# Optimization experiments

Measured on AMD Instinct MI355X. Metric: run time of the kernel, lower is better.

The kernel has to match this reference:

```python
import jax, jax.numpy as jnp
import numpy as np

NUM_LEVELS = 4
RADIUS = 4


def _bilinear_zeros(img, x, y):
    """Bilinear sample img (N,H,W) at absolute pixel coords x,y (N,S,S),
    zeros padding outside, matching torch grid_sample(align_corners=True,
    padding_mode='zeros') with absolute->normalized->absolute roundtrip."""
    N, H, W = img.shape
    x0 = jnp.floor(x); y0 = jnp.floor(y)
    x1 = x0 + 1.0;     y1 = y0 + 1.0
    wx1 = x - x0; wx0 = 1.0 - wx1
    wy1 = y - y0; wy0 = 1.0 - wy1
    flat = img.reshape(N, H * W)

    def gather(xi, yi):
        valid = (xi >= 0) & (xi <= W - 1) & (yi >= 0) & (yi <= H - 1)
        xc = jnp.clip(xi, 0, W - 1).astype(jnp.int32)
        yc = jnp.clip(yi, 0, H - 1).astype(jnp.int32)
        idx = (yc * W + xc).reshape(N, -1)
        v = jnp.take_along_axis(flat, idx, axis=1).reshape(xi.shape)
        return jnp.where(valid, v, jnp.zeros((), img.dtype))

    return (wy0 * wx0 * gather(x0, y0) + wy0 * wx1 * gather(x1, y0)
            + wy1 * wx0 * gather(x0, y1) + wy1 * wx1 * gather(x1, y1))


def _avg_pool2(v):
    N, H, W = v.shape
    return v.reshape(N, H // 2, 2, W // 2, 2).mean(axis=(2, 4))


def setup_inputs() -> dict:
    key = jax.random.key(0)
    k1, k2, k3 = jax.random.split(key, 3)
    B, M, C, H, W = 2, 4096, 256, 64, 64
    fmap1 = jax.random.normal(k1, (B, M, C), dtype=jnp.float32)
    fmap2 = jax.random.normal(k2, (B, C, H, W), dtype=jnp.float32)
    u = jax.random.uniform(k3, (B, M, 2), dtype=jnp.float32)
    centroids_coords = u * jnp.array([W - 1, H - 1], dtype=jnp.float32)
    return {"fmap1": fmap1, "fmap2": fmap2, "centroids_coords": centroids_coords}


def reference(fmap1, fmap2, centroids_coords):
    B, M, C = fmap1.shape
    _, _, H, W = fmap2.shape
    side = 2 * RADIUS + 1

    # correlation volume: (B, M, H, W) -> (B*M, H, W)
    corr = jnp.einsum('bmc,bchw->bmhw', fmap1, fmap2).reshape(B * M, H, W)

    d = jnp.arange(-RADIUS, RADIUS + 1, dtype=centroids_coords.dtype)
    di, dj = jnp.meshgrid(d, d, indexing='ij')
    delta = jnp.stack([di, dj], axis=-1)  # (S, S, 2): ch0 = x-offset, ch1 = y-offset

    c = centroids_coords.reshape(B * M, 1, 1, 2)
    vol = corr
    feats = []
    for lvl in range(NUM_LEVELS):
        sc = c + delta                        # (B*M, S, S, 2)
        sampled = _bilinear_zeros(vol, sc[..., 0], sc[..., 1])
        feats.append(sampled.reshape(B, M, side * side))
        c = c / 2.0
        if lvl < NUM_LEVELS - 1:
            vol = _avg_pool2(vol)
    # (B, M, num_levels*S*S) -> (B, out_channels, M)
    return jnp.concatenate(feats, axis=-1).transpose(0, 2, 1)
```

## Files before the change

kernel.cpp:

```cpp
#include <hip/hip_runtime.h>
#include <stdint.h>
#include <stddef.h>

static constexpr int Bb = 2;
static constexpr int Mq = 4096;
static constexpr int Cc = 256;
static constexpr int Hh = 64, Ww = 64;
static constexpr int Np = Hh * Ww;
static constexpr int RAD = 4;
static constexpr int SIDE = 2 * RAD + 1;
static constexpr int KPL = SIDE * SIDE;
static constexpr int NLVL = 4;
static constexpr int KTOT = NLVL * KPL;

static constexpr size_t L1BUF_OFF  = 0;
static constexpr size_t WINBUF_OFF = (size_t)Bb * Mq * 1024;

typedef float floatx4 __attribute__((ext_vector_type(4)));
typedef short shortx8 __attribute__((ext_vector_type(8)));

union BfPack {
    shortx8 v;
    unsigned short u[8];
};

__device__ __forceinline__ unsigned short f2bf(float f) {
    unsigned int x = __float_as_uint(f);
    x += 0x7fffu + ((x >> 16) & 1u);
    return (unsigned short)(x >> 16);
}

__device__ __forceinline__ int ksw(int row, int g) {
    return 8 * (g ^ ((row >> 1) & 3));
}

__global__ __launch_bounds__(256)
void corr_gemm_pool_kernel(const float* __restrict__ A,
                           const float* __restrict__ B2,
                           const float* __restrict__ cent,
                           float* __restrict__ l1buf,
                           float* __restrict__ winbuf)
{
    __shared__ unsigned short la[128 * 32];
    __shared__ unsigned short lb[128 * 32];
    __shared__ float corrT[32 * 129];
    __shared__ int   qx0s[128], qy0s[128];

    const int b    = blockIdx.z;
    const int bm0  = blockIdx.y * 128;
    const int bx   = blockIdx.x;
    const int bn0  = bx * 128;
    const int tid  = threadIdx.x;
    const int lane = tid & 63;
    const int wave = tid >> 6;
    const int lane15 = lane & 15;
    const int quad   = lane >> 4;
    const int wm = (wave >> 1) * 64;
    const int wn = (wave & 1) * 64;

    if (tid < 128) {
        const float cx = cent[(size_t)(b * Mq + bm0 + tid) * 2 + 0];
        const float cy = cent[(size_t)(b * Mq + bm0 + tid) * 2 + 1];
        qx0s[tid] = (int)floorf(cx) - RAD;
        qy0s[tid] = (int)floorf(cy) - RAD;
    }

    const float* Abase = A + (size_t)(b * Mq + bm0) * Cc;
    const float* Bbase = B2 + (size_t)b * Cc * Np + bn0;

    floatx4 acc[4][4];
#pragma unroll
    for (int i = 0; i < 4; ++i)
#pragma unroll
        for (int j = 0; j < 4; ++j)
            acc[i][j] = floatx4{0.0f, 0.0f, 0.0f, 0.0f};

    const int a_row = tid >> 2;
    const int a_g   = tid & 3;
    const int b_n   = tid & 127;
    const int b_g0  = tid >> 7;

    for (int k0 = 0; k0 < Cc; k0 += 32) {
        __syncthreads();
#pragma unroll
        for (int r = 0; r < 2; ++r) {
            const int row = a_row + r * 64;
            const float* src = Abase + (size_t)row * Cc + k0 + a_g * 8;
            const float4 v0 = *(const float4*)(src);
            const float4 v1 = *(const float4*)(src + 4);
            BfPack p;
            p.u[0] = f2bf(v0.x); p.u[1] = f2bf(v0.y);
            p.u[2] = f2bf(v0.z); p.u[3] = f2bf(v0.w);
            p.u[4] = f2bf(v1.x); p.u[5] = f2bf(v1.y);
            p.u[6] = f2bf(v1.z); p.u[7] = f2bf(v1.w);
            *(shortx8*)&la[row * 32 + ksw(row, a_g)] = p.v;
        }
#pragma unroll
        for (int r = 0; r < 2; ++r) {
            const int g = b_g0 + r * 2;
            const float* src = Bbase + (size_t)(k0 + g * 8) * Np + b_n;
            BfPack p;
#pragma unroll
            for (int u = 0; u < 8; ++u)
                p.u[u] = f2bf(src[(size_t)u * Np]);
            *(shortx8*)&lb[b_n * 32 + ksw(b_n, g)] = p.v;
        }
        __syncthreads();
        shortx8 af[4], bf[4];
#pragma unroll
        for (int i = 0; i < 4; ++i) {
            const int row = wm + i * 16 + lane15;
            af[i] = *(const shortx8*)&la[row * 32 + ksw(row, quad)];
        }
#pragma unroll
        for (int j = 0; j < 4; ++j) {
            const int nn = wn + j * 16 + lane15;
            bf[j] = *(const shortx8*)&lb[nn * 32 + ksw(nn, quad)];
        }
#pragma unroll
        for (int i = 0; i < 4; ++i)
#pragma unroll
            for (int j = 0; j < 4; ++j)
                acc[i][j] = __builtin_amdgcn_mfma_f32_16x16x32_bf16(
                    af[i], bf[j], acc[i][j], 0, 0, 0);
    }

    const int m_local = tid >> 3;
    const int xi      = tid & 7;
#pragma unroll
    for (int c = 0; c < 4; ++c) {
        __syncthreads();
        if ((wave >> 1) == (c >> 1)) {
#pragma unroll
            for (int ii = 0; ii < 2; ++ii) {
                const int i = 2 * (c & 1) + ii;
#pragma unroll
                for (int j = 0; j < 4; ++j) {
#pragma unroll
                    for (int reg = 0; reg < 4; ++reg) {
                        const int rl = ii * 16 + quad * 4 + reg;
                        const int n  = wn + j * 16 + lane15;
                        corrT[rl * 129 + n] = acc[i][j][reg];
                    }
                }
            }
        }
        __syncthreads();

        const int mg = 32 * c + m_local;
        const size_t gq = (size_t)(b * Mq + bm0 + mg);
        const float* T = &corrT[m_local * 129];

#pragma unroll
        for (int k = 0; k < 4; ++k) {
            const int c1 = xi + 8 * k;
            const float v = 0.25f * (T[2 * c1] + T[2 * c1 + 1]
                                   + T[64 + 2 * c1] + T[64 + 2 * c1 + 1]);
            l1buf[gq * 1024 + bx * 32 + c1] = v;
        }

        const int x0w = qx0s[mg];
        const int y0w = qy0s[mg];
#pragma unroll
        for (int par = 0; par < 2; ++par) {
            const int wy = 2 * bx + par - y0w;
            if (wy >= 0 && wy < 10) {
#pragma unroll
                for (int t = 0; t < 2; ++t) {
                    const int wx = xi + t * 8;
                    if (wx < 10) {
                        const int x = x0w + wx;
                        if (x >= 0 && x < Ww)
                            winbuf[gq * 100 + wy * 10 + wx] = T[par * 64 + x];
                    }
                }
            }
        }
    }
}

__global__ __launch_bounds__(256)
void pyr_sample_kernel(const float* __restrict__ cent,
                       const float* __restrict__ l1buf,
                       const float* __restrict__ winbuf,
                       float* __restrict__ out)
{
    __shared__ float l1[8][1024];
    __shared__ float l2[8][256];
    __shared__ float l3[8][64];
    __shared__ float win0[8][100];
    __shared__ float qcx[8], qcy[8];
    __shared__ int   qx0[8], qy0[8];

    const int tid = threadIdx.x;
    const int b   = blockIdx.x >> 9;
    const int m0  = (blockIdx.x & 511) * 8;
    const size_t gq0 = (size_t)(b * Mq + m0);

    if (tid < 8) {
        const float cx = cent[(gq0 + tid) * 2 + 0];
        const float cy = cent[(gq0 + tid) * 2 + 1];
        qcx[tid] = cx; qcy[tid] = cy;
        qx0[tid] = (int)floorf(cx) - RAD;
        qy0[tid] = (int)floorf(cy) - RAD;
    }

#pragma unroll
    for (int it = 0; it < 8; ++it) {
        const int v = it * 256 + tid;
        const int q = v >> 8;
        const int o = v & 255;
        *(float4*)&l1[q][o * 4] = *(const float4*)&l1buf[(gq0 + q) * 1024 + o * 4];
    }
    if (tid < 200) {
        const int q = tid / 25;
        const int o = tid - q * 25;
        *(float4*)&win0[q][o * 4] = *(const float4*)&winbuf[(gq0 + q) * 100 + o * 4];
    }
    __syncthreads();

#pragma unroll
    for (int i = 0; i < 8; ++i) {
        const int idx = i * 256 + tid;
        const int q = idx >> 8;
        const int c = idx & 255;
        const int cy2 = c >> 4, cx2 = c & 15;
        const float* s = &l1[q][(2 * cy2) * 32 + 2 * cx2];
        l2[q][c] = 0.25f * (s[0] + s[1] + s[32] + s[33]);
    }
    __syncthreads();
#pragma unroll
    for (int i = 0; i < 2; ++i) {
        const int idx = i * 256 + tid;
        const int q = idx >> 6;
        const int c = idx & 63;
        const int cy3 = c >> 3, cx3 = c & 7;
        const float* s = &l2[q][(2 * cy3) * 16 + 2 * cx3];
        l3[q][c] = 0.25f * (s[0] + s[1] + s[16] + s[17]);
    }
    __syncthreads();

    for (int i = 0; i < 11; ++i) {
        const int idx = i * 256 + tid;
        if (idx >= KTOT * 8) break;
        const int q  = idx & 7;
        const int kk = idx >> 3;
        const int lvl = kk / KPL;
        const int r   = kk - lvl * KPL;
        const int di  = r / SIDE;
        const int dj  = r - di * SIDE;

        const int w = Ww >> lvl;
        const float scale = 1.0f / (float)(1 << lvl);
        const float x = qcx[q] * scale + (float)(di - RAD);
        const float y = qcy[q] * scale + (float)(dj - RAD);

        const float x0f = floorf(x), y0f = floorf(y);
        const float wx1 = x - x0f, wx0 = 1.0f - wx1;
        const float wy1 = y - y0f, wy0 = 1.0f - wy1;
        const float fmx = (float)(w - 1);
        const bool vx0 = (x0f >= 0.0f) && (x0f <= fmx);
        const bool vx1 = (x0f + 1.0f >= 0.0f) && (x0f + 1.0f <= fmx);
        const bool vy0 = (y0f >= 0.0f) && (y0f <= fmx);
        const bool vy1 = (y0f + 1.0f >= 0.0f) && (y0f + 1.0f <= fmx);

        const int ix0 = (int)x0f, iy0 = (int)y0f;

        const float* buf;
        int stride, ox, oy;
        if (lvl == 0)      { buf = win0[q]; stride = 10; ox = qx0[q]; oy = qy0[q]; }
        else if (lvl == 1) { buf = l1[q];   stride = 32; ox = 0; oy = 0; }
        else if (lvl == 2) { buf = l2[q];   stride = 16; ox = 0; oy = 0; }
        else               { buf = l3[q];   stride =  8; ox = 0; oy = 0; }

        const int cx0 = ix0 - ox, cx1 = ix0 + 1 - ox;
        const int cy0r = iy0 - oy, cy1r = iy0 + 1 - oy;
        const float g00 = (vx0 && vy0) ? buf[cy0r * stride + cx0] : 0.0f;
        const float g10 = (vx1 && vy0) ? buf[cy0r * stride + cx1] : 0.0f;
        const float g01 = (vx0 && vy1) ? buf[cy1r * stride + cx0] : 0.0f;
        const float g11 = (vx1 && vy1) ? buf[cy1r * stride + cx1] : 0.0f;

        out[((size_t)b * KTOT + kk) * Mq + m0 + q] =
            wy0 * (wx0 * g00 + wx1 * g10) + wy1 * (wx0 * g01 + wx1 * g11);
    }
}

extern "C" void kernel_launch(void* const* d_in, const int* in_sizes, int n_in,
                              void* d_out, int out_size, void* d_ws, size_t ws_size,
                              hipStream_t stream)
{
    const float* fmap1 = (const float*)d_in[0];
    const float* fmap2 = (const float*)d_in[1];
    const float* cent  = (const float*)d_in[2];
    float* l1buf  = (float*)d_ws + L1BUF_OFF;
    float* winbuf = (float*)d_ws + WINBUF_OFF;
    float* out = (float*)d_out;

    dim3 ggrid(Np / 128, Mq / 128, Bb);
    corr_gemm_pool_kernel<<<ggrid, 256, 0, stream>>>(fmap1, fmap2, cent,
                                                     l1buf, winbuf);

    const int nblk = Bb * Mq / 8;
    pyr_sample_kernel<<<nblk, 256, 0, stream>>>(cent, l1buf, winbuf, out);
}
```

Before: 129.0 us.

## Pre-convert inputs to bf16 and stream GEMM tiles via global_load_lds

Adds two pre-pass kernels that convert fmap1 to bf16 and transpose-convert fmap2 to a K-contiguous bf16 layout in workspace. The GEMM then loads tiles directly into LDS with global_load_lds instead of doing per-element strided fp32 loads and conversions in every block, which were repeated across many blocks. LDS for the staging tiles and the corrT transpose buffer is unioned, and the corrT stride changes. The cost is two extra launches and extra workspace traffic, and the XOR swizzle on the LDS tiles is dropped, which may bring back bank conflicts on the fragment reads.

```diff
diff --git a/kernel.cpp b/kernel.cpp
--- a/kernel.cpp
+++ b/kernel.cpp
@@ -13,8 +13,10 @@
 static constexpr int NLVL = 4;
 static constexpr int KTOT = NLVL * KPL;
 
-static constexpr size_t L1BUF_OFF  = 0;
-static constexpr size_t WINBUF_OFF = (size_t)Bb * Mq * 1024;
+static constexpr size_t L1BUF_B  = 0;
+static constexpr size_t WINBUF_B = (size_t)Bb * Mq * 1024 * 4;
+static constexpr size_t ABF_B    = WINBUF_B + (size_t)Bb * Mq * 100 * 4;
+static constexpr size_t BT_B     = ABF_B + (size_t)Bb * Mq * Cc * 2;
 
 typedef float floatx4 __attribute__((ext_vector_type(4)));
 typedef short shortx8 __attribute__((ext_vector_type(8)));
@@ -30,21 +32,68 @@
     return (unsigned short)(x >> 16);
 }
 
-__device__ __forceinline__ int ksw(int row, int g) {
-    return 8 * (g ^ ((row >> 1) & 3));
+__device__ __forceinline__ void gll16(const void* g, void* l) {
+    __builtin_amdgcn_global_load_lds(
+        (const __attribute__((address_space(1))) unsigned int*)g,
+        (__attribute__((address_space(3))) unsigned int*)l, 16, 0, 0);
 }
 
 __global__ __launch_bounds__(256)
-void corr_gemm_pool_kernel(const float* __restrict__ A,
-                           const float* __restrict__ B2,
+void cvt_a_kernel(const float* __restrict__ in, unsigned short* __restrict__ out)
+{
+    const int t = blockIdx.x * blockDim.x + threadIdx.x;
+    const float4 v0 = *(const float4*)(in + (size_t)t * 8);
+    const float4 v1 = *(const float4*)(in + (size_t)t * 8 + 4);
+    BfPack p;
+    p.u[0] = f2bf(v0.x); p.u[1] = f2bf(v0.y);
+    p.u[2] = f2bf(v0.z); p.u[3] = f2bf(v0.w);
+    p.u[4] = f2bf(v1.x); p.u[5] = f2bf(v1.y);
+    p.u[6] = f2bf(v1.z); p.u[7] = f2bf(v1.w);
+    *(shortx8*)(out + (size_t)t * 8) = p.v;
+}
+
+__global__ __launch_bounds__(256)
+void cvt_bt_kernel(const float* __restrict__ in, unsigned short* __restrict__ out)
+{
+    __shared__ float tile[64 * 65];
+    const int p0 = blockIdx.x * 64;
+    const int c0 = blockIdx.y * 64;
+    const int b  = blockIdx.z;
+    const int tid = threadIdx.x;
+
+    const int pl = tid & 63;
+    const int cb = tid >> 6;
+#pragma unroll
+    for (int it = 0; it < 16; ++it) {
+        const int cl = it * 4 + cb;
+        tile[cl * 65 + pl] = in[((size_t)(b * Cc + c0 + cl)) * Np + p0 + pl];
+    }
+    __syncthreads();
+
+    const int cg = (tid & 7) * 8;
+#pragma unroll
+    for (int it = 0; it < 2; ++it) {
+        const int pw = it * 32 + (tid >> 3);
+        BfPack p;
+#pragma unroll
+        for (int u = 0; u < 8; ++u)
+            p.u[u] = f2bf(tile[(cg + u) * 65 + pw]);
+        *(shortx8*)(out + ((size_t)(b * Np + p0 + pw)) * Cc + c0 + cg) = p.v;
+    }
+}
+
+__global__ __launch_bounds__(256)
+void corr_gemm_pool_kernel(const unsigned short* __restrict__ Abf,
+                           const unsigned short* __restrict__ Bt,
                            const float* __restrict__ cent,
                            float* __restrict__ l1buf,
                            float* __restrict__ winbuf)
 {
-    __shared__ unsigned short la[128 * 32];
-    __shared__ unsigned short lb[128 * 32];
-    __shared__ float corrT[32 * 129];
-    __shared__ int   qx0s[128], qy0s[128];
+    __shared__ union {
+        struct { unsigned short la[128 * 32]; unsigned short lb[128 * 32]; } t;
+        float corrT[32 * 130];
+    } sm;
+    __shared__ int qx0s[128], qy0s[128];
 
     const int b    = blockIdx.z;
     const int bm0  = blockIdx.y * 128;
@@ -65,8 +114,13 @@
         qy0s[tid] = (int)floorf(cy) - RAD;
     }
 
-    const float* Abase = A + (size_t)(b * Mq + bm0) * Cc;
-    const float* Bbase = B2 + (size_t)b * Cc * Np + bn0;
+    unsigned short* la = sm.t.la;
+    unsigned short* lb = sm.t.lb;
+
+    const int lrow = lane >> 2;
+    const int lkg  = (lane & 3) * 8;
+    const unsigned short* aptr = Abf + (size_t)(b * Mq + bm0 + wave * 16 + lrow) * Cc + lkg;
+    const unsigned short* bptr = Bt  + (size_t)(b * Np + bn0 + wave * 16 + lrow) * Cc + lkg;
 
     floatx4 acc[4][4];
 #pragma unroll
@@ -75,48 +129,21 @@
         for (int j = 0; j < 4; ++j)
             acc[i][j] = floatx4{0.0f, 0.0f, 0.0f, 0.0f};
 
-    const int a_row = tid >> 2;
-    const int a_g   = tid & 3;
-    const int b_n   = tid & 127;
-    const int b_g0  = tid >> 7;
-
     for (int k0 = 0; k0 < Cc; k0 += 32) {
         __syncthreads();
-#pragma unroll
-        for (int r = 0; r < 2; ++r) {
-            const int row = a_row + r * 64;
-            const float* src = Abase + (size_t)row * Cc + k0 + a_g * 8;
-            const float4 v0 = *(const float4*)(src);
-            const float4 v1 = *(const float4*)(src + 4);
-            BfPack p;
-            p.u[0] = f2bf(v0.x); p.u[1] = f2bf(v0.y);
-            p.u[2] = f2bf(v0.z); p.u[3] = f2bf(v0.w);
-            p.u[4] = f2bf(v1.x); p.u[5] = f2bf(v1.y);
-            p.u[6] = f2bf(v1.z); p.u[7] = f2bf(v1.w);
-            *(shortx8*)&la[row * 32 + ksw(row, a_g)] = p.v;
-        }
-#pragma unroll
-        for (int r = 0; r < 2; ++r) {
-            const int g = b_g0 + r * 2;
-            const float* src = Bbase + (size_t)(k0 + g * 8) * Np + b_n;
-            BfPack p;
-#pragma unroll
-            for (int u = 0; u < 8; ++u)
-                p.u[u] = f2bf(src[(size_t)u * Np]);
-            *(shortx8*)&lb[b_n * 32 + ksw(b_n, g)] = p.v;
-        }
+        gll16(aptr + k0,            &la[wave * 512]);
+        gll16(aptr + 64 * Cc + k0,  &la[2048 + wave * 512]);
+        gll16(bptr + k0,            &lb[wave * 512]);
+        gll16(bptr + 64 * Cc + k0,  &lb[2048 + wave * 512]);
         __syncthreads();
+
         shortx8 af[4], bf[4];
 #pragma unroll
-        for (int i = 0; i < 4; ++i) {
-            const int row = wm + i * 16 + lane15;
-            af[i] = *(const shortx8*)&la[row * 32 + ksw(row, quad)];
-        }
-#pragma unroll
-        for (int j = 0; j < 4; ++j) {
-            const int nn = wn + j * 16 + lane15;
-            bf[j] = *(const shortx8*)&lb[nn * 32 + ksw(nn, quad)];
-        }
+        for (int i = 0; i < 4; ++i)
+            af[i] = *(const shortx8*)&la[(wm + i * 16 + lane15) * 32 + quad * 8];
+#pragma unroll
+        for (int j = 0; j < 4; ++j)
+            bf[j] = *(const shortx8*)&lb[(wn + j * 16 + lane15) * 32 + quad * 8];
 #pragma unroll
         for (int i = 0; i < 4; ++i)
 #pragma unroll
@@ -125,6 +152,7 @@
                     af[i], bf[j], acc[i][j], 0, 0, 0);
     }
 
+    float* corrT = sm.corrT;
     const int m_local = tid >> 3;
     const int xi      = tid & 7;
 #pragma unroll
@@ -140,7 +168,7 @@
                     for (int reg = 0; reg < 4; ++reg) {
                         const int rl = ii * 16 + quad * 4 + reg;
                         const int n  = wn + j * 16 + lane15;
-                        corrT[rl * 129 + n] = acc[i][j][reg];
+                        corrT[rl * 130 + n] = acc[i][j][reg];
                     }
                 }
             }
@@ -149,7 +177,7 @@
 
         const int mg = 32 * c + m_local;
         const size_t gq = (size_t)(b * Mq + bm0 + mg);
-        const float* T = &corrT[m_local * 129];
+        const float* T = &corrT[m_local * 130];
 
 #pragma unroll
         for (int k = 0; k < 4; ++k) {
@@ -292,13 +320,19 @@
     const float* fmap1 = (const float*)d_in[0];
     const float* fmap2 = (const float*)d_in[1];
     const float* cent  = (const float*)d_in[2];
-    float* l1buf  = (float*)d_ws + L1BUF_OFF;
-    float* winbuf = (float*)d_ws + WINBUF_OFF;
+    char* ws = (char*)d_ws;
+    float* l1buf  = (float*)(ws + L1BUF_B);
+    float* winbuf = (float*)(ws + WINBUF_B);
+    unsigned short* Abf = (unsigned short*)(ws + ABF_B);
+    unsigned short* Bt  = (unsigned short*)(ws + BT_B);
     float* out = (float*)d_out;
 
+    cvt_a_kernel<<<Bb * Mq * Cc / (8 * 256), 256, 0, stream>>>(fmap1, Abf);
+    dim3 tgrid(Np / 64, Cc / 64, Bb);
+    cvt_bt_kernel<<<tgrid, 256, 0, stream>>>(fmap2, Bt);
+
     dim3 ggrid(Np / 128, Mq / 128, Bb);
-    corr_gemm_pool_kernel<<<ggrid, 256, 0, stream>>>(fmap1, fmap2, cent,
-                                                     l1buf, winbuf);
+    corr_gemm_pool_kernel<<<ggrid, 256, 0, stream>>>(Abf, Bt, cent, l1buf, winbuf);
 
     const int nblk = Bb * Mq / 8;
     pyr_sample_kernel<<<nblk, 256, 0, stream>>>(cent, l1buf, winbuf, out);
```

Result: no change. 128.7 us (-0.2%).
